# Kernel optimization log

Hardware: AMD Instinct MI355X
Metric: run time of the kernel (lower is better)

Reference implementation:

```python
import jax, jax.numpy as jnp
import numpy as np

DIM = 1024
HEADS = 16


def setup_inputs() -> dict:
    key = jax.random.key(0)
    ks = jax.random.split(key, 5)
    x = jax.random.normal(ks[0], (2, 2048, DIM), dtype=jnp.float32)
    # nn.Linear init-like scaling
    qkv_w = jax.random.normal(ks[1], (3 * DIM, DIM), dtype=jnp.float32) * (1.0 / np.sqrt(DIM))
    qkv_b = jax.random.normal(ks[2], (3 * DIM,), dtype=jnp.float32) * 0.02
    proj_w = jax.random.normal(ks[3], (DIM, DIM), dtype=jnp.float32) * (1.0 / np.sqrt(DIM))
    proj_b = jax.random.normal(ks[4], (DIM,), dtype=jnp.float32) * 0.02
    return {"x": x, "qkv_w": qkv_w, "qkv_b": qkv_b, "proj_w": proj_w, "proj_b": proj_b}


def reference(x, qkv_w, qkv_b, proj_w, proj_b):
    B, N, C = x.shape
    H = HEADS
    Dh = C // H
    scale = Dh ** -0.5
    # qkv: [B, N, 3C] -> [3, B, H, N, Dh]
    qkv = (x @ qkv_w.T + qkv_b).reshape(B, N, 3, H, Dh).transpose(2, 0, 3, 1, 4)
    q, k, v = qkv[0], qkv[1], qkv[2]
    attn = jnp.einsum('bhnd,bhmd->bhnm', q, k) * scale
    attn = jax.nn.softmax(attn, axis=-1)
    out = jnp.einsum('bhnm,bhmd->bhnd', attn, v)  # [B, H, N, Dh]
    out = out.transpose(0, 2, 1, 3).reshape(B, N, C)
    return out @ proj_w.T + proj_b
```

## Files before the change

kernel.cpp:

```cpp
#include <hip/hip_runtime.h>
#include <stdint.h>

#define DIM    1024
#define NHEADS 16
#define DH     64
#define SEQ    2048
#define BATCH  2
#define BHEADS (BATCH * NHEADS)
#define MROWS  (BATCH * SEQ)
#define SL2E   0.18033688011112042f

typedef __attribute__((ext_vector_type(8))) short bf16x8;
typedef __attribute__((ext_vector_type(4))) float f32x4;
typedef unsigned short ushort_t;

#define GLDS(gp, lp) __builtin_amdgcn_global_load_lds( \
    (__attribute__((address_space(1))) void*)(gp), \
    (__attribute__((address_space(3))) void*)(lp), 16, 0, 0)

__device__ inline ushort_t f2bf(float f) {
    unsigned u = __builtin_bit_cast(unsigned, f);
    u += 0x7FFFu + ((u >> 16) & 1u);
    return (ushort_t)(u >> 16);
}

__global__ __launch_bounds__(256) void cvt_kernel(
    const float* __restrict__ s0, const float* __restrict__ s1, const float* __restrict__ s2,
    ushort_t* __restrict__ d0, ushort_t* __restrict__ d1, ushort_t* __restrict__ d2)
{
    const int N0 = MROWS * DIM;
    const int N1 = 3 * DIM * DIM;
    const int N2 = DIM * DIM;
    int e = (blockIdx.x * 256 + threadIdx.x) << 2;
    const float* src; ushort_t* dst;
    if (e < N0)                { src = s0 + e;             dst = d0 + e; }
    else if (e < N0 + N1)      { src = s1 + (e - N0);      dst = d1 + (e - N0); }
    else if (e < N0 + N1 + N2) { src = s2 + (e - N0 - N1); dst = d2 + (e - N0 - N1); }
    else return;
    float4 f = *(const float4*)src;
    ushort4 o;
    o.x = f2bf(f.x); o.y = f2bf(f.y); o.z = f2bf(f.z); o.w = f2bf(f.w);
    *(ushort4*)dst = o;
}

__global__ __launch_bounds__(256) void qkv_gemm(
    const ushort_t* __restrict__ A, const ushort_t* __restrict__ W,
    const float* __restrict__ bias,
    ushort_t* __restrict__ Qw, ushort_t* __restrict__ Kw, ushort_t* __restrict__ Vt)
{
    __shared__ ushort_t smem[128 * 136];
    ushort_t* As = smem;
    ushort_t* Bs = smem + 128 * 64;

    const int tid  = threadIdx.x;
    const int lane = tid & 63;
    const int wave = tid >> 6;
    const int quad = lane >> 4;
    const int l16  = lane & 15;
    const int wm   = (wave >> 1) * 64;
    const int wn   = (wave & 1) * 64;
    const int bm   = blockIdx.x * 128;
    const int bn   = blockIdx.y * 128;
    const int Rl   = lane >> 3;
    const int pp   = lane & 7;

    f32x4 acc[4][4];
    for (int i = 0; i < 4; i++)
        for (int j = 0; j < 4; j++)
            for (int r = 0; r < 4; r++) acc[i][j][r] = 0.f;

    for (int kk = 0; kk < DIM; kk += 64) {
        __syncthreads();
        for (int j = 0; j < 4; j++) {
            int Rb = j * 32 + wave * 8;
            int R  = Rb + Rl;
            int c  = pp ^ (R & 7);
            GLDS(A + (size_t)(bm + R) * DIM + kk + c * 8, As + Rb * 64 + lane * 8);
            GLDS(W + (size_t)(bn + R) * DIM + kk + c * 8, Bs + Rb * 64 + lane * 8);
        }
        __syncthreads();

        for (int kh = 0; kh < 2; kh++) {
            bf16x8 a[4], b[4];
            for (int mi = 0; mi < 4; mi++) {
                int r = wm + mi * 16 + l16;
                a[mi] = *(const bf16x8*)(As + r * 64 + (((kh * 4 + quad) ^ (r & 7)) << 3));
            }
            for (int ni = 0; ni < 4; ni++) {
                int r = wn + ni * 16 + l16;
                b[ni] = *(const bf16x8*)(Bs + r * 64 + (((kh * 4 + quad) ^ (r & 7)) << 3));
            }
            for (int mi = 0; mi < 4; mi++)
                for (int ni = 0; ni < 4; ni++)
                    acc[mi][ni] = __builtin_amdgcn_mfma_f32_16x16x32_bf16(a[mi], b[ni], acc[mi][ni], 0, 0, 0);
        }
    }

    __syncthreads();
    const int three = bn >> 10;
    const float scale = (three == 0) ? SL2E : 1.0f;
    for (int ni = 0; ni < 4; ni++) {
        int cl   = wn + ni * 16 + l16;
        float bv = bias[bn + cl];
        for (int mi = 0; mi < 4; mi++)
            for (int reg = 0; reg < 4; reg++) {
                int r = wm + mi * 16 + quad * 4 + reg;
                smem[r * 136 + cl] = f2bf((acc[mi][ni][reg] + bv) * scale);
            }
    }
    __syncthreads();

    const int b = bm >> 11, npos0 = bm & 2047;
    if (three < 2) {
        int r = tid >> 1, hh = tid & 1;
        int hc = (bn + hh * 64) & 1023;
        int h  = hc >> 6;
        ushort_t* dst = (three == 0 ? Qw : Kw) + ((size_t)(b * NHEADS + h) * SEQ + npos0 + r) * DH;
        const ushort_t* srcp = smem + r * 136 + hh * 64;
        for (int s = 0; s < 8; s++)
            *(uint4*)(dst + s * 8) = *(const uint4*)(srcp + s * 8);
    } else {
        int c = tid & 127, hh = tid >> 7;
        int hc = (bn + c) & 1023;
        int h  = hc >> 6, d = hc & 63;
        ushort_t* dst = Vt + ((size_t)(b * NHEADS + h) * DH + d) * SEQ + npos0 + hh * 64;
        for (int s = 0; s < 8; s++) {
            union { ushort_t u[8]; uint4 v; } tmp;
            for (int k2 = 0; k2 < 8; k2++)
                tmp.u[k2] = smem[(hh * 64 + s * 8 + k2) * 136 + c];
            *(uint4*)(dst + s * 8) = tmp.v;
        }
    }
}

__global__ __launch_bounds__(512, 4) void attn_kernel(
    const ushort_t* __restrict__ Qw, const ushort_t* __restrict__ Kw,
    const ushort_t* __restrict__ Vt, ushort_t* __restrict__ Ao)
{
    __shared__ ushort_t KV[3][2][64 * 64];
    __shared__ ushort_t QP[8 * 32 * 64];

    const int tid  = threadIdx.x;
    const int lane = tid & 63;
    const int wave = tid >> 6;
    const int quad = lane >> 4;
    const int l16  = lane & 15;
    const int bh   = blockIdx.y;
    const int q0   = blockIdx.x * 256;
    const int Rl   = lane >> 3;
    const int pp   = lane & 7;

    const ushort_t* Qh = Qw + (size_t)bh * SEQ * DH;
    const ushort_t* Kh = Kw + (size_t)bh * SEQ * DH;
    const ushort_t* Vh = Vt + (size_t)bh * DH * SEQ;

    for (int j = 0; j < 4; j++) {
        int Rb = j * 64 + wave * 8;
        int R  = Rb + Rl;
        int c  = pp ^ (R & 7);
        GLDS(Qh + (size_t)(q0 + R) * DH + c * 8, QP + Rb * 64 + lane * 8);
    }
    for (int t = 0; t < 2; t++) {
        int Rb = wave * 8;
        int R  = Rb + Rl;
        int c  = pp ^ (R & 7);
        GLDS(Kh + (size_t)(t * 64 + R) * DH + c * 8,  KV[t][0] + Rb * 64 + lane * 8);
        GLDS(Vh + (size_t)R * SEQ + t * 64 + c * 8,   KV[t][1] + Rb * 64 + lane * 8);
    }
    __syncthreads();

    bf16x8 qf[2][2];
    for (int mi = 0; mi < 2; mi++)
        for (int kh = 0; kh < 2; kh++) {
            int r = wave * 32 + mi * 16 + l16;
            qf[mi][kh] = *(const bf16x8*)(QP + r * 64 + (((kh * 4 + quad) ^ (r & 7)) << 3));
        }
    __syncthreads();

    bf16x8 vones;
    for (int i = 0; i < 8; i++) vones[i] = (short)0x3F80;

    f32x4 oacc[2][4], liacc[2];
    for (int mi = 0; mi < 2; mi++) {
        for (int r = 0; r < 4; r++) liacc[mi][r] = 0.f;
        for (int d = 0; d < 4; d++)
            for (int r = 0; r < 4; r++) oacc[mi][d][r] = 0.f;
    }

    ushort_t* Pw = QP + wave * 32 * 64;

    const int NT = SEQ / 64;
    int cur = 0;
    for (int jt = 0; jt < NT; jt++) {
        if (jt < NT - 2) {
            int pidx = cur + 2; if (pidx >= 3) pidx -= 3;
            int nj0  = (jt + 2) * 64;
            int Rb = wave * 8;
            int R  = Rb + Rl;
            int c  = pp ^ (R & 7);
            GLDS(Kh + (size_t)(nj0 + R) * DH + c * 8,  KV[pidx][0] + Rb * 64 + lane * 8);
            GLDS(Vh + (size_t)R * SEQ + nj0 + c * 8,   KV[pidx][1] + Rb * 64 + lane * 8);
        }
        const ushort_t* Ksb = KV[cur][0];
        const ushort_t* Vsb = KV[cur][1];

        f32x4 s[2][4];
        for (int mi = 0; mi < 2; mi++)
            for (int nf = 0; nf < 4; nf++)
                for (int r = 0; r < 4; r++) s[mi][nf][r] = 0.f;
        for (int kh = 0; kh < 2; kh++)
            for (int nf = 0; nf < 4; nf++) {
                int r = nf * 16 + l16;
                bf16x8 kf = *(const bf16x8*)(Ksb + r * 64 + (((kh * 4 + quad) ^ (r & 7)) << 3));
                s[0][nf] = __builtin_amdgcn_mfma_f32_16x16x32_bf16(kf, qf[0][kh], s[0][nf], 0, 0, 0);
                s[1][nf] = __builtin_amdgcn_mfma_f32_16x16x32_bf16(kf, qf[1][kh], s[1][nf], 0, 0, 0);
            }

        for (int mi = 0; mi < 2; mi++) {
            int row = mi * 16 + l16;
            for (int nf = 0; nf < 4; nf++) {
                unsigned u0 = __builtin_bit_cast(unsigned, __builtin_amdgcn_exp2f(s[mi][nf][0])) + 0x8000u;
                unsigned u1 = __builtin_bit_cast(unsigned, __builtin_amdgcn_exp2f(s[mi][nf][1])) + 0x8000u;
                unsigned u2 = __builtin_bit_cast(unsigned, __builtin_amdgcn_exp2f(s[mi][nf][2])) + 0x8000u;
                unsigned u3 = __builtin_bit_cast(unsigned, __builtin_amdgcn_exp2f(s[mi][nf][3])) + 0x8000u;
                uint2 pk;
                pk.x = __builtin_amdgcn_perm(u1, u0, 0x07060302u);
                pk.y = __builtin_amdgcn_perm(u3, u2, 0x07060302u);
                int j0 = 2 * nf + (quad >> 1);
                int jp = j0 ^ (row & 7);
                *(uint2*)(Pw + row * 64 + jp * 8 + (quad & 1) * 4) = pk;
            }
        }

        bf16x8 pf[2][2];
        for (int mi = 0; mi < 2; mi++) {
            int row = mi * 16 + l16;
            for (int kh = 0; kh < 2; kh++) {
                int jp = (kh * 4 + quad) ^ (row & 7);
                pf[mi][kh] = *(const bf16x8*)(Pw + row * 64 + jp * 8);
            }
        }

        for (int mi = 0; mi < 2; mi++) {
            liacc[mi] = __builtin_amdgcn_mfma_f32_16x16x32_bf16(pf[mi][0], vones, liacc[mi], 0, 0, 0);
            liacc[mi] = __builtin_amdgcn_mfma_f32_16x16x32_bf16(pf[mi][1], vones, liacc[mi], 0, 0, 0);
        }
        for (int kh = 0; kh < 2; kh++)
            for (int df = 0; df < 4; df++) {
                int r = df * 16 + l16;
                bf16x8 vf = *(const bf16x8*)(Vsb + r * 64 + (((kh * 4 + quad) ^ (r & 7)) << 3));
                oacc[0][df] = __builtin_amdgcn_mfma_f32_16x16x32_bf16(pf[0][kh], vf, oacc[0][df], 0, 0, 0);
                oacc[1][df] = __builtin_amdgcn_mfma_f32_16x16x32_bf16(pf[1][kh], vf, oacc[1][df], 0, 0, 0);
            }

        if (jt < NT - 2) {
            __asm volatile("s_waitcnt vmcnt(2)" ::: "memory");
        } else {
            __asm volatile("s_waitcnt vmcnt(0)" ::: "memory");
        }
        __asm volatile("s_barrier" ::: "memory");

        cur++; if (cur == 3) cur = 0;
    }

    const int b = bh >> 4, h = bh & 15;
    for (int mi = 0; mi < 2; mi++)
        for (int r = 0; r < 4; r++) {
            float inv = 1.0f / liacc[mi][r];
            int row = q0 + wave * 32 + mi * 16 + quad * 4 + r;
            for (int df = 0; df < 4; df++) {
                int col = h * 64 + df * 16 + l16;
                Ao[((size_t)b * SEQ + row) * DIM + col] = f2bf(oacc[mi][df][r] * inv);
            }
        }
}

__global__ __launch_bounds__(256, 4) void proj_gemm(
    const ushort_t* __restrict__ A, const ushort_t* __restrict__ W,
    const float* __restrict__ bias, float* __restrict__ Cout)
{
    __shared__ ushort_t As[128 * 64];
    __shared__ ushort_t Bs[64 * 64];

    const int tid  = threadIdx.x;
    const int lane = tid & 63;
    const int wave = tid >> 6;
    const int quad = lane >> 4;
    const int l16  = lane & 15;
    const int wm   = (wave >> 1) * 64;
    const int wn   = (wave & 1) * 32;
    const int bm   = blockIdx.x * 128;
    const int bn   = blockIdx.y * 64;
    const int Rl   = lane >> 3;
    const int pp   = lane & 7;

    f32x4 acc[4][2];
    for (int i = 0; i < 4; i++)
        for (int j = 0; j < 2; j++)
            for (int r = 0; r < 4; r++) acc[i][j][r] = 0.f;

    for (int kk = 0; kk < DIM; kk += 64) {
        __syncthreads();
        for (int j = 0; j < 4; j++) {
            int Rb = j * 32 + wave * 8;
            int R  = Rb + Rl;
            int c  = pp ^ (R & 7);
            GLDS(A + (size_t)(bm + R) * DIM + kk + c * 8, As + Rb * 64 + lane * 8);
        }
        for (int j = 0; j < 2; j++) {
            int Rb = j * 32 + wave * 8;
            int R  = Rb + Rl;
            int c  = pp ^ (R & 7);
            GLDS(W + (size_t)(bn + R) * DIM + kk + c * 8, Bs + Rb * 64 + lane * 8);
        }
        __syncthreads();

        for (int kh = 0; kh < 2; kh++) {
            bf16x8 a[4], b[2];
            for (int mi = 0; mi < 4; mi++) {
                int r = wm + mi * 16 + l16;
                a[mi] = *(const bf16x8*)(As + r * 64 + (((kh * 4 + quad) ^ (r & 7)) << 3));
            }
            for (int ni = 0; ni < 2; ni++) {
                int r = wn + ni * 16 + l16;
                b[ni] = *(const bf16x8*)(Bs + r * 64 + (((kh * 4 + quad) ^ (r & 7)) << 3));
            }
            for (int mi = 0; mi < 4; mi++)
                for (int ni = 0; ni < 2; ni++)
                    acc[mi][ni] = __builtin_amdgcn_mfma_f32_16x16x32_bf16(a[mi], b[ni], acc[mi][ni], 0, 0, 0);
        }
    }

    for (int mi = 0; mi < 4; mi++) {
        for (int ni = 0; ni < 2; ni++) {
            int col  = bn + wn + ni * 16 + l16;
            float bv = bias[col];
            for (int reg = 0; reg < 4; reg++) {
                int row = bm + wm + mi * 16 + quad * 4 + reg;
                Cout[(size_t)row * DIM + col] = acc[mi][ni][reg] + bv;
            }
        }
    }
}

extern "C" void kernel_launch(void* const* d_in, const int* in_sizes, int n_in,
                              void* d_out, int out_size, void* d_ws, size_t ws_size,
                              hipStream_t stream) {
    const float* x      = (const float*)d_in[0];
    const float* qkv_w  = (const float*)d_in[1];
    const float* qkv_b  = (const float*)d_in[2];
    const float* proj_w = (const float*)d_in[3];
    const float* proj_b = (const float*)d_in[4];
    float* out = (float*)d_out;

    ushort_t* xb      = (ushort_t*)d_ws;
    ushort_t* qkv_wb  = xb      + (size_t)MROWS * DIM;
    ushort_t* proj_wb = qkv_wb  + (size_t)3 * DIM * DIM;
    ushort_t* Qw      = proj_wb + (size_t)DIM * DIM;
    ushort_t* Kw      = Qw      + (size_t)BHEADS * SEQ * DH;
    ushort_t* Vt      = Kw      + (size_t)BHEADS * SEQ * DH;
    ushort_t* Ao      = Vt      + (size_t)BHEADS * SEQ * DH;

    const int total_cvt = MROWS * DIM + 3 * DIM * DIM + DIM * DIM;
    cvt_kernel<<<total_cvt / (4 * 256), 256, 0, stream>>>(x, qkv_w, proj_w, xb, qkv_wb, proj_wb);
    qkv_gemm<<<dim3(MROWS / 128, (3 * DIM) / 128), 256, 0, stream>>>(xb, qkv_wb, qkv_b, Qw, Kw, Vt);
    attn_kernel<<<dim3(SEQ / 256, BHEADS), 512, 0, stream>>>(Qw, Kw, Vt, Ao);
    proj_gemm<<<dim3(MROWS / 128, DIM / 64), 256, 0, stream>>>(Ao, proj_wb, proj_b, out);
}
```

Measured before the change: 203.0 us.

## Double-buffer A tiles in LDS and read weight fragments straight from global

Both the QKV and projection GEMMs now keep only the activation tile in LDS, split into two buffers. The next K-slice is prefetched while the current one is multiplied, so each K step needs one barrier instead of two. Weight fragments are loaded per lane directly from global memory into registers, relying on L1/L2 caching across waves. The QKV kernel also gains a 4-blocks-per-CU occupancy hint. The trade-off is that global-load latency for the weights now sits right before the MFMAs with no prefetch, and waves sharing a column range re-read the same weight rows.

```diff
diff --git a/kernel.cpp b/kernel.cpp
--- a/kernel.cpp
+++ b/kernel.cpp
@@ -43,14 +43,12 @@
     *(ushort4*)dst = o;
 }
 
-__global__ __launch_bounds__(256) void qkv_gemm(
+__global__ __launch_bounds__(256, 4) void qkv_gemm(
     const ushort_t* __restrict__ A, const ushort_t* __restrict__ W,
     const float* __restrict__ bias,
     ushort_t* __restrict__ Qw, ushort_t* __restrict__ Kw, ushort_t* __restrict__ Vt)
 {
     __shared__ ushort_t smem[128 * 136];
-    ushort_t* As = smem;
-    ushort_t* Bs = smem + 128 * 64;
 
     const int tid  = threadIdx.x;
     const int lane = tid & 63;
@@ -69,26 +67,39 @@
         for (int j = 0; j < 4; j++)
             for (int r = 0; r < 4; r++) acc[i][j][r] = 0.f;
 
-    for (int kk = 0; kk < DIM; kk += 64) {
+    const ushort_t* Wr[4];
+    for (int ni = 0; ni < 4; ni++)
+        Wr[ni] = W + (size_t)(bn + wn + ni * 16 + l16) * DIM;
+
+    const int NIT = DIM / 64;
+    for (int j = 0; j < 4; j++) {
+        int Rb = wave * 32 + j * 8;
+        int R  = Rb + Rl;
+        int c  = pp ^ (R & 7);
+        GLDS(A + (size_t)(bm + R) * DIM + c * 8, smem + Rb * 64 + lane * 8);
+    }
+
+    for (int it = 0; it < NIT; it++) {
         __syncthreads();
-        for (int j = 0; j < 4; j++) {
-            int Rb = j * 32 + wave * 8;
-            int R  = Rb + Rl;
-            int c  = pp ^ (R & 7);
-            GLDS(A + (size_t)(bm + R) * DIM + kk + c * 8, As + Rb * 64 + lane * 8);
-            GLDS(W + (size_t)(bn + R) * DIM + kk + c * 8, Bs + Rb * 64 + lane * 8);
-        }
-        __syncthreads();
-
+        ushort_t* Asb = smem + (it & 1) * (128 * 64);
+        if (it + 1 < NIT) {
+            ushort_t* Asn = smem + ((it + 1) & 1) * (128 * 64);
+            int kk = (it + 1) * 64;
+            for (int j = 0; j < 4; j++) {
+                int Rb = wave * 32 + j * 8;
+                int R  = Rb + Rl;
+                int c  = pp ^ (R & 7);
+                GLDS(A + (size_t)(bm + R) * DIM + kk + c * 8, Asn + Rb * 64 + lane * 8);
+            }
+        }
+        int kk = it * 64;
         for (int kh = 0; kh < 2; kh++) {
             bf16x8 a[4], b[4];
+            for (int ni = 0; ni < 4; ni++)
+                b[ni] = *(const bf16x8*)(Wr[ni] + kk + kh * 32 + quad * 8);
             for (int mi = 0; mi < 4; mi++) {
                 int r = wm + mi * 16 + l16;
-                a[mi] = *(const bf16x8*)(As + r * 64 + (((kh * 4 + quad) ^ (r & 7)) << 3));
-            }
-            for (int ni = 0; ni < 4; ni++) {
-                int r = wn + ni * 16 + l16;
-                b[ni] = *(const bf16x8*)(Bs + r * 64 + (((kh * 4 + quad) ^ (r & 7)) << 3));
+                a[mi] = *(const bf16x8*)(Asb + r * 64 + (((kh * 4 + quad) ^ (r & 7)) << 3));
             }
             for (int mi = 0; mi < 4; mi++)
                 for (int ni = 0; ni < 4; ni++)
@@ -279,8 +290,7 @@
     const ushort_t* __restrict__ A, const ushort_t* __restrict__ W,
     const float* __restrict__ bias, float* __restrict__ Cout)
 {
-    __shared__ ushort_t As[128 * 64];
-    __shared__ ushort_t Bs[64 * 64];
+    __shared__ ushort_t As[2][128 * 64];
 
     const int tid  = threadIdx.x;
     const int lane = tid & 63;
@@ -299,31 +309,39 @@
         for (int j = 0; j < 2; j++)
             for (int r = 0; r < 4; r++) acc[i][j][r] = 0.f;
 
-    for (int kk = 0; kk < DIM; kk += 64) {
+    const ushort_t* Wr[2];
+    for (int ni = 0; ni < 2; ni++)
+        Wr[ni] = W + (size_t)(bn + wn + ni * 16 + l16) * DIM;
+
+    const int NIT = DIM / 64;
+    for (int j = 0; j < 4; j++) {
+        int Rb = wave * 32 + j * 8;
+        int R  = Rb + Rl;
+        int c  = pp ^ (R & 7);
+        GLDS(A + (size_t)(bm + R) * DIM + c * 8, As[0] + Rb * 64 + lane * 8);
+    }
+
+    for (int it = 0; it < NIT; it++) {
         __syncthreads();
-        for (int j = 0; j < 4; j++) {
-            int Rb = j * 32 + wave * 8;
-            int R  = Rb + Rl;
-            int c  = pp ^ (R & 7);
-            GLDS(A + (size_t)(bm + R) * DIM + kk + c * 8, As + Rb * 64 + lane * 8);
-        }
-        for (int j = 0; j < 2; j++) {
-            int Rb = j * 32 + wave * 8;
-            int R  = Rb + Rl;
-            int c  = pp ^ (R & 7);
-            GLDS(W + (size_t)(bn + R) * DIM + kk + c * 8, Bs + Rb * 64 + lane * 8);
-        }
-        __syncthreads();
-
+        const ushort_t* Asb = As[it & 1];
+        if (it + 1 < NIT) {
+            ushort_t* Asn = As[(it + 1) & 1];
+            int kk = (it + 1) * 64;
+            for (int j = 0; j < 4; j++) {
+                int Rb = wave * 32 + j * 8;
+                int R  = Rb + Rl;
+                int c  = pp ^ (R & 7);
+                GLDS(A + (size_t)(bm + R) * DIM + kk + c * 8, Asn + Rb * 64 + lane * 8);
+            }
+        }
+        int kk = it * 64;
         for (int kh = 0; kh < 2; kh++) {
             bf16x8 a[4], b[2];
+            for (int ni = 0; ni < 2; ni++)
+                b[ni] = *(const bf16x8*)(Wr[ni] + kk + kh * 32 + quad * 8);
             for (int mi = 0; mi < 4; mi++) {
                 int r = wm + mi * 16 + l16;
-                a[mi] = *(const bf16x8*)(As + r * 64 + (((kh * 4 + quad) ^ (r & 7)) << 3));
-            }
-            for (int ni = 0; ni < 2; ni++) {
-                int r = wn + ni * 16 + l16;
-                b[ni] = *(const bf16x8*)(Bs + r * 64 + (((kh * 4 + quad) ^ (r & 7)) << 3));
+                a[mi] = *(const bf16x8*)(Asb + r * 64 + (((kh * 4 + quad) ^ (r & 7)) << 3));
             }
             for (int mi = 0; mi < 4; mi++)
                 for (int ni = 0; ni < 2; ni++)
```

New measurement: 222.5 us. 9.6% more time.
